# Performance work log

Measured on AMD Instinct MI355X. Metric: run time of the kernel, lower is better.

Reference implementation:

```python
import jax, jax.numpy as jnp
import numpy as np

N = 65536      # nodes
E = 524288     # edges (avg degree 8)
C = 128        # in_channels == hidden_channels
L = 3          # num_layers
EPS = 1e-5     # BatchNorm eps


def setup_inputs() -> dict:
    key = jax.random.key(0)
    ks = jax.random.split(key, 12)
    inv = 1.0 / np.sqrt(C)
    return {
        "x": jax.random.normal(ks[0], (N, C), jnp.float32),
        "edge_weight": jax.random.uniform(ks[1], (E,), jnp.float32),
        "bn_gamma": 1.0 + 0.1 * jax.random.normal(ks[2], (L, C), jnp.float32),
        "bn_beta": 0.1 * jax.random.normal(ks[3], (L, C), jnp.float32),
        "W_self": inv * jax.random.normal(ks[4], (L, C, C), jnp.float32),
        "W_neigh": inv * jax.random.normal(ks[5], (L, C, C), jnp.float32),
        "bias": 0.01 * jax.random.normal(ks[6], (L, C), jnp.float32),
        "lin_w": inv * jax.random.normal(ks[7], (C,), jnp.float32),
        "lin_b": 0.01 * jax.random.normal(ks[8], (), jnp.float32),
        "src": jax.random.randint(ks[9], (E,), 0, N),
        "dst": jax.random.randint(ks[10], (E,), 0, N),
    }


def reference(x, edge_weight, bn_gamma, bn_beta, W_self, W_neigh, bias, lin_w, lin_b, src, dst):
    # log1p on edge weights (done once in the torch module per layer; identical each layer)
    ew = jnp.log1p(edge_weight)[:, None]                     # [E,1]
    # in-degree for mean aggregation (DGL fn.mean); isolated nodes -> divide by 1 (sum is 0)
    deg = jax.ops.segment_sum(jnp.ones((E,), x.dtype), dst, num_segments=N)
    deg = jnp.maximum(deg, 1.0)[:, None]                     # [N,1]

    h = x
    for l in range(L):
        # BatchNorm1d over nodes (training-mode batch stats, biased variance)
        mu = jnp.mean(h, axis=0)
        var = jnp.mean((h - mu) ** 2, axis=0)
        h = (h - mu) * jax.lax.rsqrt(var + EPS) * bn_gamma[l] + bn_beta[l]
        # SAGEConv mean aggregator: msg = h[src] * w, neigh = mean over in-edges
        msg = h[src] * ew                                    # [E,C]
        neigh = jax.ops.segment_sum(msg, dst, num_segments=N) / deg  # [N,C]
        h = jax.nn.relu(h @ W_self[l] + neigh @ W_neigh[l] + bias[l])
    return h @ lin_w + lin_b                                 # [N]
```

## Files before the change

### kernel.cpp

```cpp
#include <hip/hip_runtime.h>
#include <hip/hip_fp16.h>

#define NN 65536
#define EE 524288
#define CC 128
#define CAP 32
#define RPB 64
#define NBUCK 8

typedef _Float16 f16x8 __attribute__((ext_vector_type(8)));
typedef float f32x4 __attribute__((ext_vector_type(4)));


__global__ void k_init(const float* __restrict__ x, __half* __restrict__ h,
                       float* __restrict__ pstat0,
                       const int* __restrict__ src, const int* __restrict__ dst,
                       const float* __restrict__ ew,
                       int* __restrict__ cnt, unsigned int* __restrict__ buf) {
    int b = blockIdx.x, t = threadIdx.x;
    if (b < 256) {
        const float4* xv = (const float4*)x;
        __half2* o = (__half2*)h;
        float s[4] = {0, 0, 0, 0}, q[4] = {0, 0, 0, 0};
        for (int k = 0; k < 32; k++) {
            int i = b * 8192 + k * 256 + t;
            float4 v = xv[i];
            o[2 * i]     = __floats2half2_rn(v.x, v.y);
            o[2 * i + 1] = __floats2half2_rn(v.z, v.w);
            s[0] += v.x; s[1] += v.y; s[2] += v.z; s[3] += v.w;
            q[0] += v.x * v.x; q[1] += v.y * v.y; q[2] += v.z * v.z; q[3] += v.w * v.w;
        }
        __shared__ float ls[256];
        ls[t] = 0.f;
        __syncthreads();
        int c0 = (t & 31) * 4;
#pragma unroll
        for (int u = 0; u < 4; u++) {
            atomicAdd(&ls[c0 + u], s[u]);
            atomicAdd(&ls[128 + c0 + u], q[u]);
        }
        __syncthreads();
        if (t < 128) {
            atomicAdd(&pstat0[t], ls[t]);
            atomicAdd(&pstat0[128 + t], ls[128 + t]);
        }
    } else {
        int base = (b - 256) * 1024 + t;
        int dd[4], sr[4];
        float we[4];
#pragma unroll
        for (int u = 0; u < 4; u++) dd[u] = dst[base + u * 256];
#pragma unroll
        for (int u = 0; u < 4; u++) sr[u] = src[base + u * 256];
#pragma unroll
        for (int u = 0; u < 4; u++) we[u] = ew[base + u * 256];
        int pos[4];
#pragma unroll
        for (int u = 0; u < 4; u++) pos[u] = atomicAdd(&cnt[dd[u]], 1);
#pragma unroll
        for (int u = 0; u < 4; u++) {
            float w = log1pf(we[u]);
            unsigned int pk = (unsigned int)sr[u] |
                              ((unsigned int)__half_as_ushort(__float2half(w)) << 16);
            if (pos[u] < CAP) buf[dd[u] * CAP + pos[u]] = pk;
        }
    }
}


__global__ void k_fold(const float* __restrict__ pstat_l,
                       const float* __restrict__ gamma, const float* __restrict__ beta,
                       const float* __restrict__ Ws, const float* __restrict__ Wn,
                       const float* __restrict__ bias,
                       __half* __restrict__ Wcat, float* __restrict__ crow,
                       float* __restrict__ cneigh) {
    int bid = blockIdx.x;
    int tid = threadIdx.x;
    int c = bid * 2 + (tid >> 7);
    int k = tid & 127;
    float su = 0.f, sq = 0.f;
#pragma unroll
    for (int b = 0; b < NBUCK; b++) {
        su += pstat_l[b * 256 + k];
        sq += pstat_l[b * 256 + 128 + k];
    }
    float mu = su * (1.0f / NN);
    float var = sq * (1.0f / NN) - mu * mu;
    float alpha = rsqrtf(var + 1e-5f) * gamma[k];
    float delta = beta[k] - mu * alpha;
    float ws = Ws[k * 128 + c];
    float wn = Wn[k * 128 + c];
    Wcat[c * 256 + k]       = __float2half(alpha * ws);
    Wcat[c * 256 + 128 + k] = __float2half(alpha * wn);
    float rs = delta * ws, rn = delta * wn;
#pragma unroll
    for (int off = 1; off < 64; off <<= 1) {
        rs += __shfl_xor(rs, off);
        rn += __shfl_xor(rn, off);
    }
    __shared__ float tmp[8];
    int wv = tid >> 6;
    if ((tid & 63) == 0) { tmp[wv * 2] = rs; tmp[wv * 2 + 1] = rn; }
    __syncthreads();
    if ((tid & 127) == 0) {
        int base = (tid >> 7) * 4;
        crow[c]   = bias[c] + tmp[base + 0] + tmp[base + 2];
        cneigh[c] = tmp[base + 1] + tmp[base + 3];
    }
}

__launch_bounds__(256, 4)
__global__ void k_layer(const __half* __restrict__ hin,
                        const int* __restrict__ cnt,
                        const unsigned int* __restrict__ buf,
                        const __half* __restrict__ Wcat,
                        const float* __restrict__ crow, const float* __restrict__ cneigh,
                        float* __restrict__ sod, int writeSod,
                        const float* __restrict__ lin_w, const float* __restrict__ lin_b,
                        __half* __restrict__ hout, float* __restrict__ outv, int mode,
                        float* __restrict__ pstatN) {
    __shared__ __half aggT[RPB * 136];
    __shared__ float sodT[RPB];
    int tid = threadIdx.x;
    int lane = tid & 63;
    int wvid = tid >> 6;
    int l15 = lane & 15, quad = lane >> 4;
    int i0 = blockIdx.x * RPB;
    int rbase = i0 + wvid * 16;

    f16x8 as0[4];
#pragma unroll
    for (int s = 0; s < 4; s++) {
        int kof = s * 32 + quad * 8;
        as0[s] = *(const f16x8*)&hin[(rbase + l15) * 128 + kof];
    }

    const f16x8* hv = (const f16x8*)hin;
    int dv = cnt[rbase + l15]; if (dv > CAP) dv = CAP;
    unsigned int pkg0, pkg1, pkg2, pkg3;
    pkg0 = buf[(rbase + 0 * 4 + quad) * CAP + l15];
    pkg1 = buf[(rbase + 1 * 4 + quad) * CAP + l15];
    pkg2 = buf[(rbase + 2 * 4 + quad) * CAP + l15];
    pkg3 = buf[(rbase + 3 * 4 + quad) * CAP + l15];

#pragma unroll
    for (int g = 0; g < 4; g++) {
        unsigned int pk = (g == 0) ? pkg0 : (g == 1) ? pkg1 : (g == 2) ? pkg2 : pkg3;
        int dq = __shfl(dv, g * 4 + quad);
        int t0 = __shfl_xor(dq, 16); int dm = dq > t0 ? dq : t0;
        int t1 = __shfl_xor(dm, 32); dm = dm > t1 ? dm : t1;
        unsigned int pk2 = 0;
        if (dm > 16) pk2 = buf[(rbase + g * 4 + quad) * CAP + 16 + l15];
        float acc[8];
#pragma unroll
        for (int u = 0; u < 8; u++) acc[u] = 0.f;
        int nch = (dm + 7) >> 3;
        for (int c = 0; c < nch; ++c) {
            unsigned int sreg = (c & 2) ? pk2 : pk;
            int sbase = (quad << 4) + ((c & 1) << 3);
            int e0 = c * 8;
            unsigned int pe[8];
#pragma unroll
            for (int e = 0; e < 8; e++) pe[e] = __shfl(sreg, sbase + e);
#pragma unroll
            for (int e = 0; e < 8; e++) if (e0 + e >= dq) pe[e] = 0;
            f16x8 ve[8];
#pragma unroll
            for (int e = 0; e < 8; e++) ve[e] = hv[(pe[e] & 0xFFFF) * 16 + l15];
#pragma unroll
            for (int e = 0; e < 8; e++) {
                float w = (e0 + e < dq)
                    ? __half2float(__ushort_as_half((unsigned short)(pe[e] >> 16))) : 0.f;
#pragma unroll
                for (int u = 0; u < 8; u++) acc[u] += w * (float)ve[e][u];
            }
        }
        float inv = 1.0f / (float)(dq > 1 ? dq : 1);
        int rloc = wvid * 16 + g * 4 + quad;
        f16x8 o;
#pragma unroll
        for (int u = 0; u < 8; u++) o[u] = (_Float16)(acc[u] * inv);
        *(f16x8*)&aggT[rloc * 136 + l15 * 8] = o;
        if (writeSod) {
            float ws = (l15 < dq)
                ? __half2float(__ushort_as_half((unsigned short)(pk >> 16))) : 0.f;
            if (16 + l15 < dq)
                ws += __half2float(__ushort_as_half((unsigned short)(pk2 >> 16)));
            ws += __shfl_xor(ws, 1); ws += __shfl_xor(ws, 2);
            ws += __shfl_xor(ws, 4); ws += __shfl_xor(ws, 8);
            if (l15 == 0) { sodT[rloc] = ws * inv; sod[i0 + rloc] = ws * inv; }
        }
    }

    f32x4 acc[8];
    f32x4 zero = {0.f, 0.f, 0.f, 0.f};
#pragma unroll
    for (int t = 0; t < 8; t++) acc[t] = zero;

#pragma unroll
    for (int s = 0; s < 4; s++) {
        int kof = s * 32 + quad * 8;
#pragma unroll
        for (int tn = 0; tn < 8; tn++) {
            f16x8 bf = *(const f16x8*)&Wcat[(tn * 16 + l15) * 256 + kof];
            acc[tn] = __builtin_amdgcn_mfma_f32_16x16x32_f16(as0[s], bf, acc[tn], 0, 0, 0);
        }
    }
#pragma unroll
    for (int s = 0; s < 4; s++) {
        int kof = s * 32 + quad * 8;
        f16x8 an0 = *(const f16x8*)&aggT[(wvid * 16 + l15) * 136 + kof];
#pragma unroll
        for (int tn = 0; tn < 8; tn++) {
            f16x8 bf = *(const f16x8*)&Wcat[(tn * 16 + l15) * 256 + 128 + kof];
            acc[tn] = __builtin_amdgcn_mfma_f32_16x16x32_f16(an0, bf, acc[tn], 0, 0, 0);
        }
    }

    float cr[8], cn[8];
#pragma unroll
    for (int tn = 0; tn < 8; tn++) {
        cr[tn] = crow[tn * 16 + l15];
        cn[tn] = cneigh[tn * 16 + l15];
    }
    int rwbase = i0 + wvid * 16 + quad * 4;

    if (mode == 0) {
        float cs[8], cq[8];
#pragma unroll
        for (int tn = 0; tn < 8; tn++) { cs[tn] = 0.f; cq[tn] = 0.f; }
#pragma unroll
        for (int r = 0; r < 4; r++) {
            int row = rwbase + r;
            float sdv = writeSod ? sodT[row - i0] : sod[row];
#pragma unroll
            for (int tn = 0; tn < 8; tn++) {
                float v = acc[tn][r] + cr[tn] + sdv * cn[tn];
                v = fmaxf(v, 0.f);
                hout[row * 128 + tn * 16 + l15] = __float2half(v);
                cs[tn] += v;
                cq[tn] += v * v;
            }
        }
#pragma unroll
        for (int tn = 0; tn < 8; tn++) {
            cs[tn] += __shfl_xor(cs[tn], 16); cs[tn] += __shfl_xor(cs[tn], 32);
            cq[tn] += __shfl_xor(cq[tn], 16); cq[tn] += __shfl_xor(cq[tn], 32);
        }
        float* st = (float*)aggT;
        __syncthreads();
        st[tid] = 0.f;
        __syncthreads();
        if (lane < 16) {
#pragma unroll
            for (int tn = 0; tn < 8; tn++) {
                atomicAdd(&st[tn * 16 + l15], cs[tn]);
                atomicAdd(&st[128 + tn * 16 + l15], cq[tn]);
            }
        }
        __syncthreads();
        if (tid < 128) {
            float* pb = pstatN + ((blockIdx.x & (NBUCK - 1)) << 8);
            atomicAdd(&pb[tid], st[tid]);
            atomicAdd(&pb[128 + tid], st[128 + tid]);
        }
    } else {
        float lw[8];
#pragma unroll
        for (int tn = 0; tn < 8; tn++) lw[tn] = lin_w[tn * 16 + l15];
        float lb = lin_b[0];
#pragma unroll
        for (int r = 0; r < 4; r++) {
            int row = rwbase + r;
            float sdv = sod[row];
            float p = 0.f;
#pragma unroll
            for (int tn = 0; tn < 8; tn++) {
                float v = acc[tn][r] + cr[tn] + sdv * cn[tn];
                v = fmaxf(v, 0.f);
                p += v * lw[tn];
            }
            p += __shfl_xor(p, 1);
            p += __shfl_xor(p, 2);
            p += __shfl_xor(p, 4);
            p += __shfl_xor(p, 8);
            if (l15 == 0) outv[row] = p + lb;
        }
    }
}


extern "C" void kernel_launch(void* const* d_in, const int* in_sizes, int n_in,
                              void* d_out, int out_size, void* d_ws, size_t ws_size,
                              hipStream_t stream) {
    (void)in_sizes; (void)n_in; (void)out_size; (void)ws_size;
    const float* x     = (const float*)d_in[0];
    const float* ew    = (const float*)d_in[1];
    const float* gamma = (const float*)d_in[2];
    const float* beta  = (const float*)d_in[3];
    const float* Ws    = (const float*)d_in[4];
    const float* Wn    = (const float*)d_in[5];
    const float* bias  = (const float*)d_in[6];
    const float* lin_w = (const float*)d_in[7];
    const float* lin_b = (const float*)d_in[8];
    const int*   srcI  = (const int*)d_in[9];
    const int*   dstI  = (const int*)d_in[10];
    float* out = (float*)d_out;

    char* p = (char*)d_ws;
    __half* ha   = (__half*)p; p += (size_t)NN * CC * 2;
    __half* hb   = (__half*)p; p += (size_t)NN * CC * 2;
    __half* Wcat = (__half*)p; p += 256 * 128 * 2;
    float* crow   = (float*)p; p += 512;
    float* cneigh = (float*)p; p += 512;
    float* sod    = (float*)p; p += (size_t)NN * 4;
    unsigned int* buf = (unsigned int*)p; p += (size_t)NN * CAP * 4;
    int*   cnt    = (int*)p;   p += (size_t)NN * 4;
    float* pstat  = (float*)p; p += 3 * NBUCK * 256 * 4;

    hipMemsetAsync(cnt, 0, (size_t)NN * 4 + 3 * NBUCK * 256 * 4, stream);

    k_init<<<dim3(256 + EE / 1024), dim3(256), 0, stream>>>(x, ha, pstat, srcI, dstI, ew, cnt, buf);

    const __half* hin = ha;
    __half* hout = hb;
    for (int l = 0; l < 3; l++) {
        k_fold<<<dim3(64), dim3(256), 0, stream>>>(
            pstat + (size_t)l * NBUCK * 256, gamma + l * CC, beta + l * CC,
            Ws + (size_t)l * CC * CC, Wn + (size_t)l * CC * CC, bias + l * CC,
            Wcat, crow, cneigh);
        int mode = (l == 2) ? 1 : 0;
        float* pstatN = (mode == 0) ? (pstat + (size_t)(l + 1) * NBUCK * 256) : pstat;
        k_layer<<<dim3(NN / RPB), dim3(256), 0, stream>>>(
            hin, cnt, buf, Wcat, crow, cneigh, sod, (l == 0) ? 1 : 0,
            lin_w, lin_b, hout, out, mode, pstatN);
        const __half* t = hin; hin = hout; hout = (__half*)t;
    }
}
```

Baseline: 290.7 us.

## Split fused aggregation+GEMM layer kernel into separate gather and MFMA kernels

Splits the per-layer kernel into a gather/mean-aggregation kernel that writes the aggregated features to a new fp16 global buffer, and a GEMM kernel that reads them back for the MFMA. The aggregation kernel uses one quarter-wave per node, smaller blocks and higher occupancy bounds, so it can hide more gather latency and avoid the sequential 4-group loop. This costs an extra write and read of a 16 MB intermediate per layer plus an extra launch. It also drops the shared-memory staging and one barrier in the GEMM kernel.

```diff
diff --git a/kernel.cpp b/kernel.cpp
--- a/kernel.cpp
+++ b/kernel.cpp
@@ -109,18 +109,72 @@
     }
 }
 
+__launch_bounds__(256, 6)
+__global__ void k_agg(const __half* __restrict__ hin,
+                      const int* __restrict__ cnt,
+                      const unsigned int* __restrict__ buf,
+                      __half* __restrict__ aggn, float* __restrict__ sod, int writeSod) {
+    int tid = threadIdx.x;
+    int lane = tid & 63;
+    int wvid = tid >> 6;
+    int l15 = lane & 15, quad = lane >> 4;
+    int n = blockIdx.x * 16 + wvid * 4 + quad;
+    const f16x8* hv = (const f16x8*)hin;
+
+    int d = cnt[n]; if (d > CAP) d = CAP;
+    unsigned int pk0 = 0, pk1 = 0;
+    if (l15 < d) pk0 = buf[n * CAP + l15];
+    int dm = d;
+    { int t0 = __shfl_xor(dm, 16); dm = dm > t0 ? dm : t0; }
+    { int t1 = __shfl_xor(dm, 32); dm = dm > t1 ? dm : t1; }
+    if (dm > 16 && 16 + l15 < d) pk1 = buf[n * CAP + 16 + l15];
+
+    float acc[8];
+#pragma unroll
+    for (int u = 0; u < 8; u++) acc[u] = 0.f;
+    int nch = (dm + 7) >> 3;
+    for (int c = 0; c < nch; ++c) {
+        int sbase = (quad << 4) + ((c & 1) << 3);
+        unsigned int sreg = (c & 2) ? pk1 : pk0;
+        unsigned int pe[8];
+        f16x8 ve[8];
+#pragma unroll
+        for (int e = 0; e < 8; e++) pe[e] = __shfl(sreg, sbase + e);
+#pragma unroll
+        for (int e = 0; e < 8; e++) ve[e] = hv[(pe[e] & 0xFFFF) * 16 + l15];
+#pragma unroll
+        for (int e = 0; e < 8; e++) {
+            float w = __half2float(__ushort_as_half((unsigned short)(pe[e] >> 16)));
+#pragma unroll
+            for (int u = 0; u < 8; u++) acc[u] += w * (float)ve[e][u];
+        }
+    }
+    float inv = 1.0f / (float)(d > 1 ? d : 1);
+    f16x8 o;
+#pragma unroll
+    for (int u = 0; u < 8; u++) o[u] = (_Float16)(acc[u] * inv);
+    *(f16x8*)&aggn[n * 128 + l15 * 8] = o;
+    if (writeSod) {
+        float ws = (l15 < d)
+            ? __half2float(__ushort_as_half((unsigned short)(pk0 >> 16))) : 0.f;
+        if (16 + l15 < d)
+            ws += __half2float(__ushort_as_half((unsigned short)(pk1 >> 16)));
+        ws += __shfl_xor(ws, 1); ws += __shfl_xor(ws, 2);
+        ws += __shfl_xor(ws, 4); ws += __shfl_xor(ws, 8);
+        if (l15 == 0) sod[n] = ws * inv;
+    }
+}
+
 __launch_bounds__(256, 4)
-__global__ void k_layer(const __half* __restrict__ hin,
-                        const int* __restrict__ cnt,
-                        const unsigned int* __restrict__ buf,
-                        const __half* __restrict__ Wcat,
-                        const float* __restrict__ crow, const float* __restrict__ cneigh,
-                        float* __restrict__ sod, int writeSod,
-                        const float* __restrict__ lin_w, const float* __restrict__ lin_b,
-                        __half* __restrict__ hout, float* __restrict__ outv, int mode,
-                        float* __restrict__ pstatN) {
-    __shared__ __half aggT[RPB * 136];
-    __shared__ float sodT[RPB];
+__global__ void k_gemm(const __half* __restrict__ hin,
+                       const __half* __restrict__ aggn,
+                       const __half* __restrict__ Wcat,
+                       const float* __restrict__ crow, const float* __restrict__ cneigh,
+                       const float* __restrict__ sod,
+                       const float* __restrict__ lin_w, const float* __restrict__ lin_b,
+                       __half* __restrict__ hout, float* __restrict__ outv, int mode,
+                       float* __restrict__ pstatN) {
+    __shared__ float st[256];
     int tid = threadIdx.x;
     int lane = tid & 63;
     int wvid = tid >> 6;
@@ -128,68 +182,12 @@
     int i0 = blockIdx.x * RPB;
     int rbase = i0 + wvid * 16;
 
-    f16x8 as0[4];
+    f16x8 as0[4], an0[4];
 #pragma unroll
     for (int s = 0; s < 4; s++) {
         int kof = s * 32 + quad * 8;
         as0[s] = *(const f16x8*)&hin[(rbase + l15) * 128 + kof];
-    }
-
-    const f16x8* hv = (const f16x8*)hin;
-    int dv = cnt[rbase + l15]; if (dv > CAP) dv = CAP;
-    unsigned int pkg0, pkg1, pkg2, pkg3;
-    pkg0 = buf[(rbase + 0 * 4 + quad) * CAP + l15];
-    pkg1 = buf[(rbase + 1 * 4 + quad) * CAP + l15];
-    pkg2 = buf[(rbase + 2 * 4 + quad) * CAP + l15];
-    pkg3 = buf[(rbase + 3 * 4 + quad) * CAP + l15];
-
-#pragma unroll
-    for (int g = 0; g < 4; g++) {
-        unsigned int pk = (g == 0) ? pkg0 : (g == 1) ? pkg1 : (g == 2) ? pkg2 : pkg3;
-        int dq = __shfl(dv, g * 4 + quad);
-        int t0 = __shfl_xor(dq, 16); int dm = dq > t0 ? dq : t0;
-        int t1 = __shfl_xor(dm, 32); dm = dm > t1 ? dm : t1;
-        unsigned int pk2 = 0;
-        if (dm > 16) pk2 = buf[(rbase + g * 4 + quad) * CAP + 16 + l15];
-        float acc[8];
-#pragma unroll
-        for (int u = 0; u < 8; u++) acc[u] = 0.f;
-        int nch = (dm + 7) >> 3;
-        for (int c = 0; c < nch; ++c) {
-            unsigned int sreg = (c & 2) ? pk2 : pk;
-            int sbase = (quad << 4) + ((c & 1) << 3);
-            int e0 = c * 8;
-            unsigned int pe[8];
-#pragma unroll
-            for (int e = 0; e < 8; e++) pe[e] = __shfl(sreg, sbase + e);
-#pragma unroll
-            for (int e = 0; e < 8; e++) if (e0 + e >= dq) pe[e] = 0;
-            f16x8 ve[8];
-#pragma unroll
-            for (int e = 0; e < 8; e++) ve[e] = hv[(pe[e] & 0xFFFF) * 16 + l15];
-#pragma unroll
-            for (int e = 0; e < 8; e++) {
-                float w = (e0 + e < dq)
-                    ? __half2float(__ushort_as_half((unsigned short)(pe[e] >> 16))) : 0.f;
-#pragma unroll
-                for (int u = 0; u < 8; u++) acc[u] += w * (float)ve[e][u];
-            }
-        }
-        float inv = 1.0f / (float)(dq > 1 ? dq : 1);
-        int rloc = wvid * 16 + g * 4 + quad;
-        f16x8 o;
-#pragma unroll
-        for (int u = 0; u < 8; u++) o[u] = (_Float16)(acc[u] * inv);
-        *(f16x8*)&aggT[rloc * 136 + l15 * 8] = o;
-        if (writeSod) {
-            float ws = (l15 < dq)
-                ? __half2float(__ushort_as_half((unsigned short)(pk >> 16))) : 0.f;
-            if (16 + l15 < dq)
-                ws += __half2float(__ushort_as_half((unsigned short)(pk2 >> 16)));
-            ws += __shfl_xor(ws, 1); ws += __shfl_xor(ws, 2);
-            ws += __shfl_xor(ws, 4); ws += __shfl_xor(ws, 8);
-            if (l15 == 0) { sodT[rloc] = ws * inv; sod[i0 + rloc] = ws * inv; }
-        }
+        an0[s] = *(const f16x8*)&aggn[(rbase + l15) * 128 + kof];
     }
 
     f32x4 acc[8];
@@ -209,11 +207,10 @@
 #pragma unroll
     for (int s = 0; s < 4; s++) {
         int kof = s * 32 + quad * 8;
-        f16x8 an0 = *(const f16x8*)&aggT[(wvid * 16 + l15) * 136 + kof];
 #pragma unroll
         for (int tn = 0; tn < 8; tn++) {
             f16x8 bf = *(const f16x8*)&Wcat[(tn * 16 + l15) * 256 + 128 + kof];
-            acc[tn] = __builtin_amdgcn_mfma_f32_16x16x32_f16(an0, bf, acc[tn], 0, 0, 0);
+            acc[tn] = __builtin_amdgcn_mfma_f32_16x16x32_f16(an0[s], bf, acc[tn], 0, 0, 0);
         }
     }
 
@@ -232,7 +229,7 @@
 #pragma unroll
         for (int r = 0; r < 4; r++) {
             int row = rwbase + r;
-            float sdv = writeSod ? sodT[row - i0] : sod[row];
+            float sdv = sod[row];
 #pragma unroll
             for (int tn = 0; tn < 8; tn++) {
                 float v = acc[tn][r] + cr[tn] + sdv * cn[tn];
@@ -247,8 +244,6 @@
             cs[tn] += __shfl_xor(cs[tn], 16); cs[tn] += __shfl_xor(cs[tn], 32);
             cq[tn] += __shfl_xor(cq[tn], 16); cq[tn] += __shfl_xor(cq[tn], 32);
         }
-        float* st = (float*)aggT;
-        __syncthreads();
         st[tid] = 0.f;
         __syncthreads();
         if (lane < 16) {
@@ -310,6 +305,7 @@
     char* p = (char*)d_ws;
     __half* ha   = (__half*)p; p += (size_t)NN * CC * 2;
     __half* hb   = (__half*)p; p += (size_t)NN * CC * 2;
+    __half* aggn = (__half*)p; p += (size_t)NN * CC * 2;
     __half* Wcat = (__half*)p; p += 256 * 128 * 2;
     float* crow   = (float*)p; p += 512;
     float* cneigh = (float*)p; p += 512;
@@ -329,10 +325,12 @@
             pstat + (size_t)l * NBUCK * 256, gamma + l * CC, beta + l * CC,
             Ws + (size_t)l * CC * CC, Wn + (size_t)l * CC * CC, bias + l * CC,
             Wcat, crow, cneigh);
+        k_agg<<<dim3(NN / 16), dim3(256), 0, stream>>>(
+            hin, cnt, buf, aggn, sod, (l == 0) ? 1 : 0);
         int mode = (l == 2) ? 1 : 0;
         float* pstatN = (mode == 0) ? (pstat + (size_t)(l + 1) * NBUCK * 256) : pstat;
-        k_layer<<<dim3(NN / RPB), dim3(256), 0, stream>>>(
-            hin, cnt, buf, Wcat, crow, cneigh, sod, (l == 0) ? 1 : 0,
+        k_gemm<<<dim3(NN / RPB), dim3(256), 0, stream>>>(
+            hin, aggn, Wcat, crow, cneigh, sod,
             lin_w, lin_b, hout, out, mode, pstatN);
         const __half* t = hin; hin = hout; hout = (__half*)t;
     }
```

Result: slower. 326.0 us (+12.1%).
